# Kernel tuning notes

Measured on AMD Instinct MI355X. Metric: run time of the kernel, lower is better.

The kernel has to match this reference:

```python
import jax, jax.numpy as jnp
import numpy as np

EPS = 1e-6

def setup_inputs() -> dict:
    key = jax.random.key(0)
    k1, k2, k3 = jax.random.split(key, 3)
    B, D, T = 4096, 4096, 16
    inputs = jax.random.normal(k1, (B, D), dtype=jnp.float32)
    W = jax.random.normal(k2, (D, T), dtype=jnp.float32)
    W_static = jax.random.normal(k3, (D, T), dtype=jnp.float32)
    return {"inputs": inputs, "W": W, "W_static": W_static}


def _znorm(A):
    # batch z-normalization per column (population std, matching tf.math.reduce_std)
    return (A - A.mean(axis=0)) / (A.std(axis=0) + EPS)


def _pls_scan(X, Ws):
    """Sequential PLS-style deflation: factor i is produced after
    orthogonalizing X against the z-normalized previous factors."""
    B = X.shape[0]
    denom = jnp.asarray(B, X.dtype)
    T = Ws.shape[1]
    cols = [X @ Ws[:, 0:1]]  # [B,1]
    for i in range(1, T):
        C = jnp.concatenate(cols, axis=1)          # [B,i]
        conv = _znorm(C)                           # [B,i]
        beta = (conv.T @ X) / denom                # [i,D]
        lin = X - conv @ beta                      # deflated inputs [B,D]
        cols.append(lin @ Ws[:, i:i + 1])
    return jnp.concatenate(cols, axis=1)           # [B,T]


def reference(inputs, W, W_static):
    # training path of FactorLayer.call
    X = _znorm(inputs)                              # batchnorm of inputs [B,D]
    c_mat = _pls_scan(X, W_static)                  # calculate_cmat with static weights
    B = X.shape[0]
    denom = jnp.asarray(B, X.dtype)
    T = W.shape[1]
    outs = [X @ W[:, 0:1]]
    for i in range(1, T):
        Cs = c_mat[:, :i]
        conv = _znorm(Cs)
        beta = (conv.T @ X) / denom                 # [i,D]
        lin = X - conv @ beta                       # training_run output [B,D]
        outs.append(lin @ W[:, i:i + 1])
    return jnp.concatenate(outs, axis=1)            # [B,T]
```

## Files before the change

kernel.cpp:

```cpp
#include <hip/hip_runtime.h>
#include <stdint.h>


#define BB 4096
#define DD 4096
#define EPSF 1e-6f

#define O_PART    0u
#define O_GRAMM   131072u
#define O_YZ      140288u
#define O_YPART   271360u

__device__ __forceinline__ int gidx(int a, int b) {
    int lo = a < b ? a : b, hi = a < b ? b : a;
    return lo * 33 + hi;
}

__global__ __launch_bounds__(256, 2)
void kA(const float* __restrict__ in, float* __restrict__ ws) {
    __shared__ float rs[8 * 132], rq[8 * 132];
    int b = blockIdx.x, t = threadIdx.x;
    int idx = b * 256 + t;
    if (idx < 8960) ws[O_GRAMM + idx] = 0.f;
    int cg = b & 31, rg = b >> 5;
    int dbase = cg * 128, r0 = rg * 256;
    int chunk = t & 31, rr = t >> 5;
    int c0 = dbase + chunk * 4;
    float s0=0.f,s1=0.f,s2=0.f,s3=0.f,q0=0.f,q1=0.f,q2=0.f,q3=0.f;
    #pragma unroll 4
    for (int i = 0; i < 32; ++i) {
        int r = r0 + i * 8 + rr;
        float4 u = *(const float4*)&in[(size_t)r * DD + c0];
        s0 += u.x; q0 += u.x*u.x;  s1 += u.y; q1 += u.y*u.y;
        s2 += u.z; q2 += u.z*u.z;  s3 += u.w; q3 += u.w*u.w;
    }
    int lb = rr * 132 + chunk * 4;
    rs[lb+0]=s0; rs[lb+1]=s1; rs[lb+2]=s2; rs[lb+3]=s3;
    rq[lb+0]=q0; rq[lb+1]=q1; rq[lb+2]=q2; rq[lb+3]=q3;
    __syncthreads();
    float* part = ws + O_PART + (size_t)rg * 8192;
    if (t < 128) {
        float a = 0.f;
        #pragma unroll
        for (int r2 = 0; r2 < 8; ++r2) a += rs[r2 * 132 + t];
        part[dbase + t] = a;
    } else {
        int ci = t - 128;
        float a = 0.f;
        #pragma unroll
        for (int r2 = 0; r2 < 8; ++r2) a += rq[r2 * 132 + ci];
        part[4096 + dbase + ci] = a;
    }
}

__global__ __launch_bounds__(256, 8)
void kB(const float* __restrict__ in, const float* __restrict__ W,
        const float* __restrict__ Wstat, float* __restrict__ ws,
        float* __restrict__ ypart) {
    __shared__ __align__(16) float tile[64 * 33];
    __shared__ __align__(16) float inv_s[128];
    int b = blockIdx.x, t = threadIdx.x;
    int dg = b & 31, rg = b >> 5;
    int dbase = dg * 128, rowbase = rg * 64;
    int chunk = t & 7, srow = t >> 3;
    int row = t & 63;
    int jq = __builtin_amdgcn_readfirstlane(t >> 6);
    const float* inp = in + (size_t)(rowbase + srow) * DD + dbase + chunk * 4;
    float4 pf0 = *(const float4*)(inp);
    float4 pf1 = *(const float4*)(inp + (size_t)32 * DD);
    {
        if (t < 128) {
            const float* part = ws + O_PART;
            float s = 0.f, q = 0.f;
            #pragma unroll
            for (int g = 0; g < 16; ++g) {
                s += part[(size_t)g * 8192 + dbase + t];
                q += part[(size_t)g * 8192 + 4096 + dbase + t];
            }
            float m = s * (1.0f / BB);
            float var = q * (1.0f / BB) - m * m; if (var < 0.f) var = 0.f;
            inv_s[t] = 1.0f / (sqrtf(var) + EPSF);
        }
        __syncthreads();
    }
    float acc[8];
    #pragma unroll
    for (int i = 0; i < 8; ++i) acc[i] = 0.f;
    const float* wbase = (jq < 2) ? (Wstat + jq * 8) : (W + (jq - 2) * 8);
    for (int stage = 0; stage < 4; ++stage) {
        int ds0 = stage * 32;
        float4 iv4 = *(const float4*)&inv_s[ds0 + chunk * 4];
        int b0 = srow * 33 + chunk * 4;
        tile[b0 + 0] = pf0.x * iv4.x; tile[b0 + 1] = pf0.y * iv4.y;
        tile[b0 + 2] = pf0.z * iv4.z; tile[b0 + 3] = pf0.w * iv4.w;
        int b1 = (srow + 32) * 33 + chunk * 4;
        tile[b1 + 0] = pf1.x * iv4.x; tile[b1 + 1] = pf1.y * iv4.y;
        tile[b1 + 2] = pf1.z * iv4.z; tile[b1 + 3] = pf1.w * iv4.w;
        __syncthreads();
        if (stage < 3) {
            pf0 = *(const float4*)(inp + (stage + 1) * 32);
            pf1 = *(const float4*)(inp + (size_t)32 * DD + (stage + 1) * 32);
        }
        const float* trow = tile + row * 33;
        #pragma unroll 4
        for (int dl = 0; dl < 32; ++dl) {
            float xs = trow[dl];
            const float* wr = wbase + (size_t)(dbase + ds0 + dl) * 16;
            #pragma unroll
            for (int j = 0; j < 8; ++j) acc[j] += xs * wr[j];
        }
        __syncthreads();
    }
    float* dst = ypart + ((size_t)dg * BB + rowbase + row) * 32 + jq * 8;
    *(float4*)(dst + 0) = make_float4(acc[0], acc[1], acc[2], acc[3]);
    *(float4*)(dst + 4) = make_float4(acc[4], acc[5], acc[6], acc[7]);
}

__global__ __launch_bounds__(256, 2)
void kC(float* __restrict__ ws) {
    __shared__ float yz_s[8 * 34];
    int b = blockIdx.x, t = threadIdx.x;
    int rowbase = b * 8;
    int r = t >> 5, c = t & 31;
    const float* yp = ws + O_YPART;
    size_t off = (size_t)(rowbase + r) * 32 + c;
    float s = 0.f;
    #pragma unroll
    for (int dg = 0; dg < 32; ++dg) s += yp[(size_t)dg * (BB * 32) + off];
    ws[O_YZ + off] = s;
    yz_s[r * 34 + c] = s;
    if (c == 0) yz_s[r * 34 + 32] = 1.0f;
    __syncthreads();
    float* gm = ws + O_GRAMM + (size_t)(b & 7) * 1120;
    for (int p = t; p < 561; p += 256) {
        int i = 0, rem = p;
        while (rem >= 33 - i) { rem -= 33 - i; ++i; }
        int j = i + rem;
        float a2 = 0.f;
        #pragma unroll
        for (int r2 = 0; r2 < 8; ++r2) a2 += yz_s[r2 * 34 + i] * yz_s[r2 * 34 + j];
        atomicAdd(&gm[i * 33 + j], a2);
    }
}

__global__ __launch_bounds__(256, 2)
void kE(const float* __restrict__ ws, float* __restrict__ out) {
    __shared__ __align__(16) float yzs[64 * 36];
    __shared__ float Sv[33], GA[17 * 17], gz[17 * 16], v[15][17], gad[15][16],
                     gzd[15][16], gu[17], u[17], st[2], wm[17 * 16];
    int b = blockIdx.x, t = threadIdx.x;
    int rowbase = b * 64;
    const float invB = 1.0f / BB;
    const float4* src = (const float4*)(ws + O_YZ) + (size_t)rowbase * 8;
    #pragma unroll
    for (int k = 0; k < 2; ++k) {
        int idx = k * 256 + t;
        float4 f = src[idx];
        int row = idx >> 3, c4 = (idx & 7) * 4;
        yzs[row * 36 + c4 + 0] = f.x; yzs[row * 36 + c4 + 1] = f.y;
        yzs[row * 36 + c4 + 2] = f.z; yzs[row * 36 + c4 + 3] = f.w;
    }
    const float* gm = ws + O_GRAMM;
    if (t < 33) {
        float s = 0.f;
        #pragma unroll
        for (int m = 0; m < 8; ++m) s += gm[m * 1120 + gidx(t, 32)];
        Sv[t] = s;
    }
    __syncthreads();
    for (int idx = t; idx < 17 * 17; idx += 256) {
        int p = idx / 17, q = idx % 17;
        float val;
        if (p < 16 && q < 16) {
            float raw = 0.f;
            #pragma unroll
            for (int m = 0; m < 8; ++m) raw += gm[m * 1120 + gidx(p, q)];
            val = raw - Sv[p] * Sv[q] * invB;
        } else if (p == 16 && q == 16) val = (float)BB;
        else val = 0.f;
        GA[idx] = val;
    }
    for (int idx = t; idx < 17 * 16; idx += 256) {
        int p = idx / 16, tt = idx % 16;
        float val = 0.f;
        if (p < 16) {
            float raw = 0.f;
            #pragma unroll
            for (int m = 0; m < 8; ++m) raw += gm[m * 1120 + gidx(p, 16 + tt)];
            val = raw - Sv[p] * Sv[16 + tt] * invB;
        }
        gz[idx] = val;
    }
    if (t < 17) u[t] = (t == 0) ? 1.f : 0.f;
    __syncthreads();
    for (int i = 0; i < 15; ++i) {
        if (t < 17) {
            float s = 0.f;
            for (int q = 0; q < 17; ++q) s += GA[t * 17 + q] * u[q];
            gu[t] = s;
        }
        __syncthreads();
        if (t == 0) {
            float mean = gu[16] * invB, e2 = 0.f;
            for (int p = 0; p < 17; ++p) e2 += u[p] * gu[p];
            e2 *= invB;
            float var = e2 - mean * mean; if (var < 0.f) var = 0.f;
            st[0] = mean; st[1] = 1.0f / (sqrtf(var) + EPSF);
        }
        __syncthreads();
        if (t < 17) v[i][t] = (u[t] - (t == 16 ? st[0] : 0.f)) * st[1];
        __syncthreads();
        if (t < 16) {
            float s = 0.f;
            for (int p = 0; p < 17; ++p) s += v[i][p] * GA[p * 17 + t];
            gad[i][t] = s;
        } else if (t < 32) {
            int tt = t - 16;
            float s = 0.f;
            for (int p = 0; p < 17; ++p) s += v[i][p] * gz[p * 16 + tt];
            gzd[i][tt] = s;
        }
        __syncthreads();
        if (t < 17) {
            float a2 = 0.f;
            for (int j = 0; j <= i; ++j) a2 += v[j][t] * gad[j][i + 1];
            u[t] = ((t == i + 1) ? 1.f : 0.f) - a2 * invB;
        }
        __syncthreads();
    }
    for (int idx = t; idx < 17 * 16; idx += 256) {
        int p = idx / 16, tt = idx % 16;
        float s = 0.f;
        for (int j = 0; j < tt; ++j) s += v[j][p] * gzd[j][tt];
        wm[idx] = s * invB;
    }
    __syncthreads();
    if (t < 16) {
        float adj = Sv[16 + t] * invB;
        for (int p = 0; p < 16; ++p) adj -= Sv[p] * invB * wm[p * 16 + t];
        wm[16 * 16 + t] += adj;
    }
    __syncthreads();
    int row = t >> 2, c0 = (t & 3) * 4;
    const float* yr = yzs + row * 36;
    float o[4];
    #pragma unroll
    for (int k = 0; k < 4; ++k) o[k] = yr[16 + c0 + k] - wm[16 * 16 + c0 + k];
    #pragma unroll
    for (int p = 0; p < 16; ++p) {
        float yp = yr[p];
        #pragma unroll
        for (int k = 0; k < 4; ++k) o[k] -= yp * wm[p * 16 + c0 + k];
    }
    *(float4*)&out[(size_t)rowbase * 16 + t * 4] = make_float4(o[0], o[1], o[2], o[3]);
}

extern "C" void kernel_launch(void* const* d_in, const int* in_sizes, int n_in,
                              void* d_out, int out_size, void* d_ws, size_t ws_size,
                              hipStream_t stream) {
    const float* in    = (const float*)d_in[0];
    const float* W     = (const float*)d_in[1];
    const float* Wstat = (const float*)d_in[2];
    float* ws  = (float*)d_ws;
    float* out = (float*)d_out;

    kA<<<dim3(512),  dim3(256), 0, stream>>>(in, ws);
    kB<<<dim3(2048), dim3(256), 0, stream>>>(in, W, Wstat, ws, ws + O_YPART);
    kC<<<dim3(512),  dim3(256), 0, stream>>>(ws);
    kE<<<dim3(64),   dim3(256), 0, stream>>>(ws, out);
}
```

Before: 149.1 us.

## Fuse partial-sum reduction and Gram accumulation into final kernel with grid barrier

Merges the kernel that reduces the per-D-group partial projections and accumulates the Gram matrix into the final solve kernel. Each of the 64 blocks now reduces 64 rows itself, atomically adds its Gram contribution, and then waits on a global atomic counter acting as a grid-wide barrier before reading the Gram sums. This removes one kernel launch and the round trip of the reduced projections through global memory. In exchange, only 64 blocks do the partial reduction, so there is less parallelism, and the spin barrier relies on all 64 blocks being resident at the same time.

```diff
diff --git a/kernel.cpp b/kernel.cpp
--- a/kernel.cpp
+++ b/kernel.cpp
@@ -8,12 +8,15 @@
 
 #define O_PART    0u
 #define O_GRAMM   131072u
-#define O_YZ      140288u
+#define O_CNT     140032u
 #define O_YPART   271360u
 
 __device__ __forceinline__ int gidx(int a, int b) {
     int lo = a < b ? a : b, hi = a < b ? b : a;
     return lo * 33 + hi;
+}
+__device__ __forceinline__ float gload(const float* p) {
+    return __hip_atomic_load(p, __ATOMIC_RELAXED, __HIP_MEMORY_SCOPE_AGENT);
 }
 
 __global__ __launch_bounds__(256, 2)
@@ -21,7 +24,7 @@
     __shared__ float rs[8 * 132], rq[8 * 132];
     int b = blockIdx.x, t = threadIdx.x;
     int idx = b * 256 + t;
-    if (idx < 8960) ws[O_GRAMM + idx] = 0.f;
+    if (idx < 8961) ws[O_GRAMM + idx] = 0.f;
     int cg = b & 31, rg = b >> 5;
     int dbase = cg * 128, r0 = rg * 256;
     int chunk = t & 31, rr = t >> 5;
@@ -117,54 +120,54 @@
 }
 
 __global__ __launch_bounds__(256, 2)
-void kC(float* __restrict__ ws) {
-    __shared__ float yz_s[8 * 34];
-    int b = blockIdx.x, t = threadIdx.x;
-    int rowbase = b * 8;
-    int r = t >> 5, c = t & 31;
-    const float* yp = ws + O_YPART;
-    size_t off = (size_t)(rowbase + r) * 32 + c;
-    float s = 0.f;
-    #pragma unroll
-    for (int dg = 0; dg < 32; ++dg) s += yp[(size_t)dg * (BB * 32) + off];
-    ws[O_YZ + off] = s;
-    yz_s[r * 34 + c] = s;
-    if (c == 0) yz_s[r * 34 + 32] = 1.0f;
-    __syncthreads();
-    float* gm = ws + O_GRAMM + (size_t)(b & 7) * 1120;
-    for (int p = t; p < 561; p += 256) {
-        int i = 0, rem = p;
-        while (rem >= 33 - i) { rem -= 33 - i; ++i; }
-        int j = i + rem;
-        float a2 = 0.f;
-        #pragma unroll
-        for (int r2 = 0; r2 < 8; ++r2) a2 += yz_s[r2 * 34 + i] * yz_s[r2 * 34 + j];
-        atomicAdd(&gm[i * 33 + j], a2);
-    }
-}
-
-__global__ __launch_bounds__(256, 2)
-void kE(const float* __restrict__ ws, float* __restrict__ out) {
+void kEF(float* __restrict__ ws, float* __restrict__ out) {
     __shared__ __align__(16) float yzs[64 * 36];
     __shared__ float Sv[33], GA[17 * 17], gz[17 * 16], v[15][17], gad[15][16],
                      gzd[15][16], gu[17], u[17], st[2], wm[17 * 16];
     int b = blockIdx.x, t = threadIdx.x;
     int rowbase = b * 64;
     const float invB = 1.0f / BB;
-    const float4* src = (const float4*)(ws + O_YZ) + (size_t)rowbase * 8;
-    #pragma unroll
-    for (int k = 0; k < 2; ++k) {
-        int idx = k * 256 + t;
-        float4 f = src[idx];
-        int row = idx >> 3, c4 = (idx & 7) * 4;
-        yzs[row * 36 + c4 + 0] = f.x; yzs[row * 36 + c4 + 1] = f.y;
-        yzs[row * 36 + c4 + 2] = f.z; yzs[row * 36 + c4 + 3] = f.w;
+    {
+        const float* yp = ws + O_YPART;
+        int r0 = t >> 5, c = t & 31;
+        for (int sweep = 0; sweep < 8; ++sweep) {
+            int r = sweep * 8 + r0;
+            size_t off = (size_t)(rowbase + r) * 32 + c;
+            float s = 0.f;
+            #pragma unroll
+            for (int dg = 0; dg < 32; ++dg) s += yp[(size_t)dg * (BB * 32) + off];
+            yzs[r * 36 + c] = s;
+            if (c == 0) yzs[r * 36 + 32] = 1.0f;
+        }
+    }
+    __syncthreads();
+    {
+        float* gm = ws + O_GRAMM + (size_t)(b & 7) * 1120;
+        for (int p = t; p < 561; p += 256) {
+            int i = 0, rem = p;
+            while (rem >= 33 - i) { rem -= 33 - i; ++i; }
+            int j = i + rem;
+            float a2 = 0.f;
+            for (int r = 0; r < 64; ++r) a2 += yzs[r * 36 + i] * yzs[r * 36 + j];
+            atomicAdd(&gm[i * 33 + j], a2);
+        }
+    }
+    __syncthreads();
+    {
+        unsigned int* cnt = (unsigned int*)(ws + O_CNT);
+        if (t == 0) {
+            __threadfence();
+            atomicAdd(cnt, 1u);
+            while (__hip_atomic_load(cnt, __ATOMIC_ACQUIRE,
+                                     __HIP_MEMORY_SCOPE_AGENT) < 64u) {}
+        }
+        __syncthreads();
     }
     const float* gm = ws + O_GRAMM;
     if (t < 33) {
         float s = 0.f;
         #pragma unroll
-        for (int m = 0; m < 8; ++m) s += gm[m * 1120 + gidx(t, 32)];
+        for (int m = 0; m < 8; ++m) s += gload(&gm[m * 1120 + gidx(t, 32)]);
         Sv[t] = s;
     }
     __syncthreads();
@@ -174,7 +177,7 @@
         if (p < 16 && q < 16) {
             float raw = 0.f;
             #pragma unroll
-            for (int m = 0; m < 8; ++m) raw += gm[m * 1120 + gidx(p, q)];
+            for (int m = 0; m < 8; ++m) raw += gload(&gm[m * 1120 + gidx(p, q)]);
             val = raw - Sv[p] * Sv[q] * invB;
         } else if (p == 16 && q == 16) val = (float)BB;
         else val = 0.f;
@@ -186,7 +189,7 @@
         if (p < 16) {
             float raw = 0.f;
             #pragma unroll
-            for (int m = 0; m < 8; ++m) raw += gm[m * 1120 + gidx(p, 16 + tt)];
+            for (int m = 0; m < 8; ++m) raw += gload(&gm[m * 1120 + gidx(p, 16 + tt)]);
             val = raw - Sv[p] * Sv[16 + tt] * invB;
         }
         gz[idx] = val;
@@ -266,6 +269,5 @@
 
     kA<<<dim3(512),  dim3(256), 0, stream>>>(in, ws);
     kB<<<dim3(2048), dim3(256), 0, stream>>>(in, W, Wstat, ws, ws + O_YPART);
-    kC<<<dim3(512),  dim3(256), 0, stream>>>(ws);
-    kE<<<dim3(64),   dim3(256), 0, stream>>>(ws, out);
-}
+    kEF<<<dim3(64),  dim3(256), 0, stream>>>(ws, out);
+}
```

After: 152.8 us. +2.4%, slower.
